# Kernel optimization log

Measured on AMD Instinct MI355X. Metric: run time of the kernel, lower is better.

## Reference

```python
import jax, jax.numpy as jnp
import numpy as np

T, B = 4096, 32
EP_LEN = 256
K = T // EP_LEN          # episodes per trajectory
LM = EP_LEN              # max episode length
S_DIM, C_DIM, M_DIM, L_DIM = 128, 32, 32, 32
E_S, E_C, H, A = 128, 64, 256, 16


def setup_inputs() -> dict:
    key = jax.random.key(0)
    ks = jax.random.split(key, 16)
    f = lambda i, shape: jax.random.normal(ks[i], shape, jnp.float32)
    inp = {
        "state": f(0, (T, B, S_DIM)),
        "latent_mean": f(1, (T, B, L_DIM)) * 0.1,
        "latent_logvar": f(2, (T, B, L_DIM)) * 0.1,
        "latent_mean_t": f(3, (T, B, L_DIM)) * 0.1,
        "latent_logvar_t": f(4, (T, B, L_DIM)) * 0.1,
        "agent_character": f(5, (T, B, C_DIM)),
        "mental_state": f(6, (T, B, M_DIM)),
        "partner_actions": jax.random.randint(ks[7], (LM, B), 0, A, jnp.int32),
    }
    # episode boundaries: done at the last step of each EP_LEN-long episode
    t = jnp.arange(T)
    inp["dones"] = jnp.broadcast_to(((t + 1) % EP_LEN == 0).astype(jnp.float32)[:, None], (T, B))
    sc = lambda fan: 1.0 / np.sqrt(fan)
    inp["W_se"] = f(8, (S_DIM, E_S)) * sc(S_DIM); inp["b_se"] = jnp.zeros((E_S,), jnp.float32)
    inp["W_ce"] = f(9, (C_DIM, E_C)) * sc(C_DIM); inp["b_ce"] = jnp.zeros((E_C,), jnp.float32)
    inp["W_sa"] = f(10, (E_S + E_C, H)) * sc(E_S + E_C); inp["b_sa"] = jnp.zeros((H,), jnp.float32)
    inp["W_h"] = f(11, (E_C + M_DIM, H)) * sc(E_C + M_DIM); inp["b_h"] = jnp.zeros((H,), jnp.float32)
    inp["Wi"] = f(12, (H, 3 * H)) * sc(H); inp["bi"] = jnp.zeros((3 * H,), jnp.float32)
    inp["Wh"] = f(13, (H, 3 * H)) * sc(H); inp["bh"] = jnp.zeros((3 * H,), jnp.float32)
    inp["W_out"] = f(14, (H, A)) * sc(H); inp["b_out"] = jnp.zeros((A,), jnp.float32)
    return inp


def _gru(h, x, Wi, bi, Wh, bh):
    gi = x @ Wi + bi
    gh = h @ Wh + bh
    ir, iz, inn = jnp.split(gi, 3, axis=-1)
    hr, hz, hn = jnp.split(gh, 3, axis=-1)
    r = jax.nn.sigmoid(ir + hr)
    z = jax.nn.sigmoid(iz + hz)
    n = jnp.tanh(inn + r * hn)
    return (1.0 - z) * n + z * h


def _episode_layout(d):  # d: [T] float dones -> (episode_id, pos_in_episode)
    started = jnp.concatenate([jnp.zeros((1,), bool), d[:-1] > 0.5])
    ep = jnp.cumsum(started.astype(jnp.int32))
    t = jnp.arange(d.shape[0])
    start = jax.lax.cummax(jnp.where(started, t, 0))
    return ep, t - start


def _to_episodes(x, ep, pos):  # x: [T, F] -> [K, LM, F]  (transform_timestep_to_batch)
    return jnp.zeros((K, LM) + x.shape[1:], x.dtype).at[ep, pos].set(x, mode="drop")


def _shift_padding_to_front(out, mask):  # out: [K, LM, D], mask: [K, LM]
    cnt = mask.sum(-1).astype(jnp.int32)
    src = jnp.arange(LM)[None, :] - (LM - cnt)[:, None]
    idx = jnp.clip(src, 0, LM - 1)
    ok = (src >= 0).astype(out.dtype)
    shifted = jnp.take_along_axis(out, idx[:, :, None], axis=1) * ok[:, :, None]
    return shifted, jnp.take_along_axis(mask, idx, axis=1) * ok


def _forward(state, latent_mean, latent_logvar, latent_mean_t, latent_logvar_t,
             agent_character, mental_state, partner_actions, dones,
             W_se, b_se, W_ce, b_ce, W_sa, b_sa, W_h, b_h, Wi, bi, Wh, bh, W_out, b_out):
    # ---- KL between consecutive-timestep posteriors ----
    lm = jnp.concatenate((latent_mean, latent_mean_t), axis=-1)
    lv = jnp.concatenate((latent_logvar, latent_logvar_t), axis=-1)
    gauss_dim = lm.shape[-1]
    all_m = jnp.concatenate((jnp.zeros((1,) + lm.shape[1:], lm.dtype), lm), axis=0)
    all_lv = jnp.concatenate((jnp.zeros((1,) + lv.shape[1:], lv.dtype), lv), axis=0)
    mu, m = all_m[1:], all_m[:-1]
    logE, logS = all_lv[1:], all_lv[:-1]
    kl = 0.5 * (jnp.sum(logS, -1) - jnp.sum(logE, -1) - gauss_dim
                + jnp.sum(jnp.exp(logE - logS), -1)
                + jnp.sum((m - mu) * (m - mu) / jnp.exp(logS), -1))  # [T,B]
    kl_loss = kl.sum(0).sum(0).mean()

    # ---- embeddings ----
    se = jax.nn.relu(state @ W_se + b_se)                         # [T,B,E_S]
    ce = jax.nn.relu(agent_character @ W_ce + b_ce)               # [T,B,E_C]
    sa = jnp.concatenate((se, ce), -1) @ W_sa + b_sa              # [T,B,H]
    hid = jnp.concatenate((ce, mental_state), -1) @ W_h + b_h     # [T,B,H]

    # ---- split trajectories into episodes (gather/scatter) ----
    ep, pos = jax.vmap(_episode_layout, in_axes=1, out_axes=0)(dones)  # [B,T] each
    to_ep = jax.vmap(_to_episodes, in_axes=(1, 0, 0), out_axes=0)
    k_sa = to_ep(sa, ep, pos)                                     # [B,K,LM,H]
    k_hid = to_ep(hid, ep, pos)                                   # [B,K,LM,H]
    k_d = to_ep(dones[..., None], ep, pos)[..., 0]                # [B,K,LM]
    mask = jax.vmap(lambda e, p: jnp.zeros((K, LM), jnp.float32).at[e, p].set(1.0, mode="drop"))(ep, pos)

    # ---- sequential RNN scan per episode (vectorized over B*K) ----
    h0 = k_hid[:, :, 0, :]                                        # [B,K,H]
    xs = (jnp.moveaxis(k_sa, 2, 0), jnp.moveaxis(k_hid, 2, 0), jnp.moveaxis(k_d, 2, 0))

    def step(h, xt):
        sa_t, hid_t, d_t = xt
        h = jnp.where(d_t[..., None] > 0.5, hid_t, h)             # reset to per-step init on done
        h = _gru(h, sa_t, Wi, bi, Wh, bh)
        return h, h

    _, ys = jax.lax.scan(step, h0, xs)                            # [LM,B,K,H]
    ys = jnp.moveaxis(ys, 0, 2)                                   # [B,K,LM,H]

    logits = (ys @ W_out + b_out) * mask[..., None]               # [B,K,LM,A]
    shifted, _ = jax.vmap(_shift_padding_to_front)(logits, mask)
    out = jnp.moveaxis(shifted.sum(1), 0, 1)                      # [LM,B,A]

    logp = jnp.take_along_axis(jax.nn.log_softmax(out, -1), partner_actions[..., None], -1)[..., 0]
    return kl_loss, logp.sum(-1)                                  # scalar, [LM]


def reference(state, latent_mean, latent_logvar, latent_mean_t, latent_logvar_t,
              agent_character, mental_state, partner_actions, dones,
              W_se, b_se, W_ce, b_ce, W_sa, b_sa, W_h, b_h, Wi, bi, Wh, bh, W_out, b_out):
    return _forward(state, latent_mean, latent_logvar, latent_mean_t, latent_logvar_t,
                    agent_character, mental_state, partner_actions, dones,
                    W_se, b_se, W_ce, b_ce, W_sa, b_sa, W_h, b_h, Wi, bi, Wh, bh, W_out, b_out)
```

## Files before the change

### kernel.cpp

```cpp
#include <hip/hip_runtime.h>
#include <math.h>

typedef short bf16x8 __attribute__((ext_vector_type(8)));
typedef float f32x4 __attribute__((ext_vector_type(4)));
typedef unsigned short u16;
typedef unsigned int u32;

#define T_DIM 4096
#define B_DIM 32

static constexpr size_t OFF_SE     = 0;
static constexpr size_t OFF_CE     = 33554432;
static constexpr size_t OFF_SA     = 50331648;
static constexpr size_t OFF_HID    = 117440512;
static constexpr size_t OFF_WHT    = 117964800;
static constexpr size_t OFF_WIT    = 118358016;
static constexpr size_t OFF_OUTACC = 118751232;
static constexpr size_t OFF_KLP    = 119799808;

__device__ __forceinline__ u16 f2bf(float x) {
    u32 b = __float_as_uint(x);
    u32 lsb = (b >> 16) & 1u;
    b += 0x7fffu + lsb;
    return (u16)(b >> 16);
}
__device__ __forceinline__ float bf2f(u16 u) {
    return __uint_as_float(((u32)u) << 16);
}
__device__ __forceinline__ float fsig(float x) {
    x = fminf(fmaxf(x, -30.f), 30.f);
    float e = __expf(x);
    return __fdividef(e, e + 1.f);
}
__device__ __forceinline__ float ftanh(float x) {
    x = fminf(fmaxf(x, -15.f), 15.f);
    float e = __expf(2.f * x);
    return __fdividef(e - 1.f, e + 1.f);
}

__global__ __launch_bounds__(256) void prep_kernel(const float* __restrict__ Wh,
                                                   const float* __restrict__ Wi,
                                                   u16* __restrict__ WhT,
                                                   u16* __restrict__ WiT) {
    int idx = blockIdx.x * 256 + threadIdx.x;
    if (idx < 196608) {
        int n = idx >> 8, k = idx & 255;
        WhT[idx] = f2bf(Wh[k * 768 + n]);
    } else {
        int i = idx - 196608;
        int n = i >> 8, k = i & 255;
        WiT[i] = f2bf(Wi[k * 768 + n]);
    }
}

#define KLTERM(MU, LE, M, LS)                   \
    do {                                        \
        float _ls = (LS), _le = (LE);           \
        sS += _ls; sE += _le;                   \
        float _es = expf(-_ls);                 \
        sX += expf(_le) * _es;                  \
        float _dm = (M) - (MU);                 \
        sQ += _dm * _dm * _es;                  \
    } while (0)

__global__ __launch_bounds__(256) void kl_kernel(const float* __restrict__ lm,
                                                 const float* __restrict__ lv,
                                                 const float* __restrict__ lmt,
                                                 const float* __restrict__ lvt,
                                                 float* __restrict__ klp) {
    __shared__ float red[256];
    int tid = threadIdx.x;
    int idx = blockIdx.x * 256 + tid;
    float sS = 0.f, sE = 0.f, sX = 0.f, sQ = 0.f;
    const int cur = idx * 32;
    const int prv = cur - B_DIM * 32;
    const bool hasprev = (idx >= B_DIM);
    for (int half = 0; half < 2; half++) {
        const float* pm = half ? lmt : lm;
        const float* pv = half ? lvt : lv;
        for (int ch = 0; ch < 8; ch++) {
            float4 mu = *(const float4*)&pm[cur + ch * 4];
            float4 le = *(const float4*)&pv[cur + ch * 4];
            float4 m = make_float4(0.f, 0.f, 0.f, 0.f);
            float4 ls = make_float4(0.f, 0.f, 0.f, 0.f);
            if (hasprev) {
                m = *(const float4*)&pm[prv + ch * 4];
                ls = *(const float4*)&pv[prv + ch * 4];
            }
            KLTERM(mu.x, le.x, m.x, ls.x);
            KLTERM(mu.y, le.y, m.y, ls.y);
            KLTERM(mu.z, le.z, m.z, ls.z);
            KLTERM(mu.w, le.w, m.w, ls.w);
        }
    }
    float kl = 0.5f * (sS - sE - 64.0f + sX + sQ);
    red[tid] = kl;
    __syncthreads();
    for (int s = 128; s > 0; s >>= 1) {
        if (tid < s) red[tid] += red[tid + s];
        __syncthreads();
    }
    if (tid == 0) klp[blockIdx.x] = red[0];
}

__global__ __launch_bounds__(256) void gemm_k(const float* __restrict__ A32a,
                                              const u16* __restrict__ A16a,
                                              const u16* __restrict__ A16b,
                                              const float* __restrict__ W,
                                              const float* __restrict__ bias,
                                              u16* __restrict__ out,
                                              int mode, int K, int N, int do_relu) {
    __shared__ __align__(16) u16 As[64 * 40];
    __shared__ __align__(16) u16 Bs[64 * 40];
    const int tid = threadIdx.x;
    const int rows0 = blockIdx.x * 64;
    const int cols0 = blockIdx.y * 64;
    const int w16 = tid >> 6;
    const int lane = tid & 63;
    const int quad = lane >> 4;
    const int l15 = lane & 15;
    f32x4 acc[4];
    for (int i = 0; i < 4; i++) acc[i] = (f32x4){0.f, 0.f, 0.f, 0.f};
    const int nsteps = K >> 5;
    const int arow = tid >> 2, aseg = (tid & 3) << 3;
    const int bk = tid >> 3, bseg = (tid & 7) << 3;
    for (int ks = 0; ks < nsteps; ks++) {
        const int grow = rows0 + arow;
        for (int j = 0; j < 8; j++) {
            const int k = ks * 32 + aseg + j;
            float v;
            if (mode == 0)      v = A32a[grow * 128 + k];
            else if (mode == 1) v = A32a[grow * 32 + k];
            else if (mode == 2) v = (k < 128) ? bf2f(A16a[grow * 128 + k])
                                              : bf2f(A16b[grow * 64 + (k - 128)]);
            else {
                const int k6 = grow >> 6, w = (grow >> 5) & 1, bb = grow & 31;
                const int trow = (k6 * 256 + w * 255) * B_DIM + bb;
                v = (k < 64) ? bf2f(A16a[trow * 64 + k]) : A32a[trow * 32 + (k - 64)];
            }
            As[arow * 40 + aseg + j] = f2bf(v);
        }
        const int gk = ks * 32 + bk;
        for (int j = 0; j < 8; j++) {
            const int c = cols0 + bseg + j;
            Bs[(bseg + j) * 40 + bk] = f2bf(W[gk * N + c]);
        }
        __syncthreads();
        bf16x8 af = *(const bf16x8*)&As[(w16 * 16 + l15) * 40 + quad * 8];
        for (int nt = 0; nt < 4; nt++) {
            bf16x8 bfr = *(const bf16x8*)&Bs[(nt * 16 + l15) * 40 + quad * 8];
            acc[nt] = __builtin_amdgcn_mfma_f32_16x16x32_bf16(af, bfr, acc[nt], 0, 0, 0);
        }
        __syncthreads();
    }
    for (int nt = 0; nt < 4; nt++) {
        const int c = cols0 + nt * 16 + l15;
        const float bv = bias[c];
        for (int r = 0; r < 4; r++) {
            const int row = rows0 + w16 * 16 + quad * 4 + r;
            float v = acc[nt][r] + bv;
            if (do_relu) v = fmaxf(v, 0.f);
            out[row * N + c] = f2bf(v);
        }
    }
}

__global__ void __launch_bounds__(256)
__attribute__((amdgpu_waves_per_eu(1, 1)))
gru5_kernel(const u16* __restrict__ hid,
            const u16* __restrict__ sa,
            const u16* __restrict__ WhT,
            const u16* __restrict__ WiT,
            const float* __restrict__ Wout,
            const float* __restrict__ bi,
            const float* __restrict__ bh,
            u16* __restrict__ gic_all,
            float* __restrict__ outacc) {
    __shared__ __align__(16) u16 whL[12 * 16 * 264];
    __shared__ __align__(16) u16 stage[64 * 264];
    __shared__ __align__(16) u16 hB[16 * 264];
    __shared__ __align__(16) u16 WoL[16 * 264];
    __shared__ float bfold[768];
    __shared__ float bhnL[256];
    const int blk = blockIdx.x;
    const int b = blk >> 1, half = blk & 1;
    const int tid = threadIdx.x;
    const int lane = tid & 63, wv = tid >> 6;
    const int quad = lane >> 4, l15 = lane & 15;
    const int sq = tid >> 5, c0 = (tid & 31) * 8;
    u16* gic = gic_all + (size_t)blk * (256 * 768);

    for (int i = tid; i < 6144; i += 256) {
        const int s = i >> 9, rr = (i >> 5) & 15, seg = (i & 31) * 8;
        const int g = (s / 3) * 12 + 9 + (s % 3);
        *(bf16x8*)&whL[(s * 16 + rr) * 264 + seg] = *(const bf16x8*)&WhT[(g * 16 + rr) * 256 + seg];
    }
    for (int i = tid; i < 4096; i += 256) {
        const int a = i >> 8, k = i & 255;
        WoL[a * 264 + k] = f2bf(Wout[k * 16 + a]);
    }
    for (int c = tid; c < 768; c += 256) bfold[c] = (c < 512) ? (bi[c] + bh[c]) : bi[c];
    if (tid < 256) bhnL[tid] = bh[512 + tid];
    float hreg[8];
    {
        bf16x8 hv = *(const bf16x8*)&hid[(size_t)((((half << 3) + sq) << 6) + b) * 256 + c0];
#pragma unroll
        for (int j = 0; j < 8; j++) hreg[j] = bf2f((u16)hv[j]);
        *(bf16x8*)&hB[sq * 264 + c0] = hv;
        bf16x8 z = (bf16x8){0, 0, 0, 0, 0, 0, 0, 0};
        *(bf16x8*)&hB[(8 + sq) * 264 + c0] = z;
    }
    __syncthreads();

    bf16x8 wreg[9][8];
    for (int ch = 0; ch < 8; ch++) {
        for (int as = 0; as < 4; as++) {
            __syncthreads();
#pragma unroll
            for (int j = 0; j < 8; j++) {
                const int lin = j * 256 + tid;
                const int row = lin >> 5, seg = (lin & 31) * 8;
                const int pcs = as * 8 + (row >> 3), sql = row & 7;
                const int t = ((half << 3) + sql) * 256 + ch * 32 + pcs;
                *(bf16x8*)&stage[row * 264 + seg] =
                    *(const bf16x8*)&sa[((size_t)(t * 32 + b)) * 256 + seg];
            }
            __syncthreads();
            bf16x8 afr[4][8];
#pragma unroll
            for (int mt = 0; mt < 4; mt++)
#pragma unroll
                for (int ks = 0; ks < 8; ks++)
                    afr[mt][ks] = *(const bf16x8*)&stage[(mt * 16 + l15) * 264 + ks * 32 + quad * 8];
            bf16x8 wc[8], wn[8];
            {
                const u16* p = &WiT[((wv * 12) * 16 + l15) * 256 + quad * 8];
#pragma unroll
                for (int ks = 0; ks < 8; ks++) wc[ks] = *(const bf16x8*)&p[ks * 32];
            }
            for (int j = 0; j < 12; j++) {
                if (j < 11) {
                    const u16* p = &WiT[((wv * 12 + j + 1) * 16 + l15) * 256 + quad * 8];
#pragma unroll
                    for (int ks = 0; ks < 8; ks++) wn[ks] = *(const bf16x8*)&p[ks * 32];
                }
                const float bf = bfold[(wv * 12 + j) * 16 + l15];
#pragma unroll
                for (int mt = 0; mt < 4; mt++) {
                    f32x4 acc = (f32x4){0.f, 0.f, 0.f, 0.f};
#pragma unroll
                    for (int ks = 0; ks < 8; ks++)
                        acc = __builtin_amdgcn_mfma_f32_16x16x32_bf16(afr[mt][ks], wc[ks], acc, 0, 0, 0);
                    const int rbase = as * 64 + mt * 16 + quad * 4;
#pragma unroll
                    for (int r = 0; r < 4; r++)
                        gic[(size_t)(rbase + r) * 768 + (wv * 12 + j) * 16 + l15] = f2bf(acc[r] + bf);
                }
#pragma unroll
                for (int ks = 0; ks < 8; ks++) wc[ks] = wn[ks];
            }
        }
#pragma unroll
        for (int j = 0; j < 9; j++) {
            const u16* p = &WhT[((wv * 12 + j) * 16 + l15) * 256 + quad * 8];
#pragma unroll
            for (int ks = 0; ks < 8; ks++) wreg[j][ks] = *(const bf16x8*)&p[ks * 32];
        }
        for (int pc = 0; pc < 32; pc++) {
            const int POS = ch * 32 + pc;
            __syncthreads();
            const u16* gp = &gic[(size_t)(pc * 8 + sq) * 768];
            bf16x8 g_r = *(const bf16x8*)&gp[c0];
            bf16x8 g_z = *(const bf16x8*)&gp[256 + c0];
            bf16x8 g_n = *(const bf16x8*)&gp[512 + c0];
            bf16x8 af[8];
            if (POS == 255) {
                const u16* hp = &hid[(size_t)((((half << 3) + (l15 & 7)) << 6) + 32 + b) * 256 + quad * 8];
#pragma unroll
                for (int ks = 0; ks < 8; ks++) af[ks] = *(const bf16x8*)&hp[ks * 32];
            } else {
#pragma unroll
                for (int ks = 0; ks < 8; ks++)
                    af[ks] = *(const bf16x8*)&hB[l15 * 264 + ks * 32 + quad * 8];
            }
            if (wv == 3 && POS > 0) {
                f32x4 acc = (f32x4){0.f, 0.f, 0.f, 0.f};
#pragma unroll
                for (int ks = 0; ks < 8; ks++) {
                    bf16x8 al = *(const bf16x8*)&hB[l15 * 264 + ks * 32 + quad * 8];
                    bf16x8 wo = *(const bf16x8*)&WoL[l15 * 264 + ks * 32 + quad * 8];
                    acc = __builtin_amdgcn_mfma_f32_16x16x32_bf16(al, wo, acc, 0, 0, 0);
                }
                float s = acc[0] + acc[1] + acc[2] + acc[3];
                s += __shfl_down(s, 32);
                s += __shfl_down(s, 16);
                if (lane < 16)
                    outacc[(size_t)half * 131072 + ((size_t)(POS - 1) * B_DIM + b) * 16 + lane] = s;
            }
#pragma unroll
            for (int j = 0; j < 9; j++) {
                f32x4 acc = (f32x4){0.f, 0.f, 0.f, 0.f};
#pragma unroll
                for (int ks = 0; ks < 8; ks++)
                    acc = __builtin_amdgcn_mfma_f32_16x16x32_bf16(af[ks], wreg[j][ks], acc, 0, 0, 0);
                const int t = wv * 12 + j;
#pragma unroll
                for (int r = 0; r < 4; r++)
                    stage[(quad * 4 + r) * 776 + t * 16 + l15] = f2bf(acc[r]);
            }
#pragma unroll
            for (int j = 9; j < 12; j++) {
                const u16* p = &whL[((wv * 3 + (j - 9)) * 16 + l15) * 264 + quad * 8];
                f32x4 acc = (f32x4){0.f, 0.f, 0.f, 0.f};
#pragma unroll
                for (int ks = 0; ks < 8; ks++)
                    acc = __builtin_amdgcn_mfma_f32_16x16x32_bf16(af[ks], *(const bf16x8*)&p[ks * 32], acc, 0, 0, 0);
                const int t = wv * 12 + j;
#pragma unroll
                for (int r = 0; r < 4; r++)
                    stage[(quad * 4 + r) * 776 + t * 16 + l15] = f2bf(acc[r]);
            }
            __syncthreads();
            if (POS == 255) {
                bf16x8 hv = *(const bf16x8*)&hid[(size_t)((((half << 3) + sq) << 6) + 32 + b) * 256 + c0];
#pragma unroll
                for (int j = 0; j < 8; j++) hreg[j] = bf2f((u16)hv[j]);
            }
            bf16x8 h_r = *(const bf16x8*)&stage[sq * 776 + c0];
            bf16x8 h_z = *(const bf16x8*)&stage[sq * 776 + 256 + c0];
            bf16x8 h_n = *(const bf16x8*)&stage[sq * 776 + 512 + c0];
            bf16x8 hp8;
#pragma unroll
            for (int j = 0; j < 8; j++) {
                const float rv = fsig(bf2f((u16)g_r[j]) + bf2f((u16)h_r[j]));
                const float zv = fsig(bf2f((u16)g_z[j]) + bf2f((u16)h_z[j]));
                const float nv = ftanh(bf2f((u16)g_n[j]) + rv * (bf2f((u16)h_n[j]) + bhnL[c0 + j]));
                hreg[j] = (1.f - zv) * nv + zv * hreg[j];
                hp8[j] = (short)f2bf(hreg[j]);
            }
            *(bf16x8*)&hB[sq * 264 + c0] = hp8;
        }
    }
    __syncthreads();
    if (wv == 3) {
        f32x4 acc = (f32x4){0.f, 0.f, 0.f, 0.f};
#pragma unroll
        for (int ks = 0; ks < 8; ks++) {
            bf16x8 al = *(const bf16x8*)&hB[l15 * 264 + ks * 32 + quad * 8];
            bf16x8 wo = *(const bf16x8*)&WoL[l15 * 264 + ks * 32 + quad * 8];
            acc = __builtin_amdgcn_mfma_f32_16x16x32_bf16(al, wo, acc, 0, 0, 0);
        }
        float s = acc[0] + acc[1] + acc[2] + acc[3];
        s += __shfl_down(s, 32);
        s += __shfl_down(s, 16);
        if (lane < 16)
            outacc[(size_t)half * 131072 + ((size_t)255 * B_DIM + b) * 16 + lane] = s;
    }
}

__global__ __launch_bounds__(64) void final_kernel(const float* __restrict__ outacc,
                                                   const int* __restrict__ pa,
                                                   const float* __restrict__ klp,
                                                   const float* __restrict__ bout,
                                                   float* __restrict__ dout) {
    const int lane = threadIdx.x;
    if (blockIdx.x == 256) {
        float s = 0.f;
        for (int j = 0; j < 8; j++) s += klp[lane + 64 * j];
        for (int off = 32; off > 0; off >>= 1) s += __shfl_down(s, off);
        if (lane == 0) dout[0] = s;
        return;
    }
    const int pos = blockIdx.x;
    float lp = 0.f;
    if (lane < 32) {
        const float* r0 = outacc + ((size_t)pos * B_DIM + lane) * 16;
        const float* r1 = r0 + 131072;
        float v[16];
        float mx = -1e30f;
#pragma unroll
        for (int a = 0; a < 16; a++) {
            v[a] = r0[a] + r1[a] + 16.0f * bout[a];
            mx = fmaxf(mx, v[a]);
        }
        float s = 0.f;
#pragma unroll
        for (int a = 0; a < 16; a++) s += expf(v[a] - mx);
        const int ai = pa[pos * B_DIM + lane];
        lp = v[ai] - mx - logf(s);
    }
    for (int off = 16; off > 0; off >>= 1) lp += __shfl_down(lp, off);
    if (lane == 0) dout[1 + pos] = lp;
}

extern "C" void kernel_launch(void* const* d_in, const int* in_sizes, int n_in,
                              void* d_out, int out_size, void* d_ws, size_t ws_size,
                              hipStream_t stream) {
    const float* state = (const float*)d_in[0];
    const float* lm    = (const float*)d_in[1];
    const float* lv    = (const float*)d_in[2];
    const float* lmt   = (const float*)d_in[3];
    const float* lvt   = (const float*)d_in[4];
    const float* ach   = (const float*)d_in[5];
    const float* ms    = (const float*)d_in[6];
    const int*   pa    = (const int*)d_in[7];
    const float* W_se  = (const float*)d_in[9];
    const float* b_se  = (const float*)d_in[10];
    const float* W_ce  = (const float*)d_in[11];
    const float* b_ce  = (const float*)d_in[12];
    const float* W_sa  = (const float*)d_in[13];
    const float* b_sa  = (const float*)d_in[14];
    const float* W_h   = (const float*)d_in[15];
    const float* b_h   = (const float*)d_in[16];
    const float* Wi    = (const float*)d_in[17];
    const float* bi    = (const float*)d_in[18];
    const float* Wh    = (const float*)d_in[19];
    const float* bh    = (const float*)d_in[20];
    const float* Wout  = (const float*)d_in[21];
    const float* bout  = (const float*)d_in[22];

    char* ws = (char*)d_ws;
    u16* se   = (u16*)(ws + OFF_SE);
    u16* ce   = (u16*)(ws + OFF_CE);
    u16* sa   = (u16*)(ws + OFF_SA);
    u16* hid  = (u16*)(ws + OFF_HID);
    u16* WhT  = (u16*)(ws + OFF_WHT);
    u16* WiT  = (u16*)(ws + OFF_WIT);
    float* outacc = (float*)(ws + OFF_OUTACC);
    float* klp    = (float*)(ws + OFF_KLP);
    float* dout   = (float*)d_out;

    prep_kernel<<<1536, 256, 0, stream>>>(Wh, Wi, WhT, WiT);
    kl_kernel<<<512, 256, 0, stream>>>(lm, lv, lmt, lvt, klp);
    gemm_k<<<dim3(2048, 2), 256, 0, stream>>>(state, nullptr, nullptr, W_se, b_se, se, 0, 128, 128, 1);
    gemm_k<<<dim3(2048, 1), 256, 0, stream>>>(ach, nullptr, nullptr, W_ce, b_ce, ce, 1, 32, 64, 1);
    gemm_k<<<dim3(2048, 4), 256, 0, stream>>>(nullptr, se, ce, W_sa, b_sa, sa, 2, 192, 256, 0);
    gemm_k<<<dim3(16, 4), 256, 0, stream>>>(ms, ce, nullptr, W_h, b_h, hid, 5, 96, 256, 0);
    gru5_kernel<<<64, 256, 0, stream>>>(hid, sa, WhT, WiT, Wout, bi, bh, se, outacc);
    final_kernel<<<257, 64, 0, stream>>>(outacc, pa, klp, bout, dout);
}
```

Measured before the change: 1.859 ms.

## Run GRU recurrence with 8 waves per block and vectorize GEMM tile loads

```diff
diff --git a/kernel.cpp b/kernel.cpp
--- a/kernel.cpp
+++ b/kernel.cpp
@@ -126,24 +126,44 @@
     const int bk = tid >> 3, bseg = (tid & 7) << 3;
     for (int ks = 0; ks < nsteps; ks++) {
         const int grow = rows0 + arow;
-        for (int j = 0; j < 8; j++) {
-            const int k = ks * 32 + aseg + j;
-            float v;
-            if (mode == 0)      v = A32a[grow * 128 + k];
-            else if (mode == 1) v = A32a[grow * 32 + k];
-            else if (mode == 2) v = (k < 128) ? bf2f(A16a[grow * 128 + k])
-                                              : bf2f(A16b[grow * 64 + (k - 128)]);
-            else {
-                const int k6 = grow >> 6, w = (grow >> 5) & 1, bb = grow & 31;
-                const int trow = (k6 * 256 + w * 255) * B_DIM + bb;
-                v = (k < 64) ? bf2f(A16a[trow * 64 + k]) : A32a[trow * 32 + (k - 64)];
-            }
-            As[arow * 40 + aseg + j] = f2bf(v);
+        const int k0 = ks * 32 + aseg;
+        if (mode == 0) {
+            float4 v0 = *(const float4*)&A32a[grow * 128 + k0];
+            float4 v1 = *(const float4*)&A32a[grow * 128 + k0 + 4];
+            u16* d = &As[arow * 40 + aseg];
+            d[0] = f2bf(v0.x); d[1] = f2bf(v0.y); d[2] = f2bf(v0.z); d[3] = f2bf(v0.w);
+            d[4] = f2bf(v1.x); d[5] = f2bf(v1.y); d[6] = f2bf(v1.z); d[7] = f2bf(v1.w);
+        } else if (mode == 1) {
+            float4 v0 = *(const float4*)&A32a[grow * 32 + k0];
+            float4 v1 = *(const float4*)&A32a[grow * 32 + k0 + 4];
+            u16* d = &As[arow * 40 + aseg];
+            d[0] = f2bf(v0.x); d[1] = f2bf(v0.y); d[2] = f2bf(v0.z); d[3] = f2bf(v0.w);
+            d[4] = f2bf(v1.x); d[5] = f2bf(v1.y); d[6] = f2bf(v1.z); d[7] = f2bf(v1.w);
+        } else if (mode == 2) {
+            bf16x8 v = (k0 < 128) ? *(const bf16x8*)&A16a[grow * 128 + k0]
+                                  : *(const bf16x8*)&A16b[grow * 64 + (k0 - 128)];
+            *(bf16x8*)&As[arow * 40 + aseg] = v;
+        } else {
+            const int k6 = grow >> 6, w = (grow >> 5) & 1, bb = grow & 31;
+            const int trow = (k6 * 256 + w * 255) * B_DIM + bb;
+            for (int j = 0; j < 8; j++) {
+                const int k = k0 + j;
+                float v = (k < 64) ? bf2f(A16a[trow * 64 + k]) : A32a[trow * 32 + (k - 64)];
+                As[arow * 40 + aseg + j] = f2bf(v);
+            }
         }
         const int gk = ks * 32 + bk;
-        for (int j = 0; j < 8; j++) {
-            const int c = cols0 + bseg + j;
-            Bs[(bseg + j) * 40 + bk] = f2bf(W[gk * N + c]);
+        {
+            float4 w0 = *(const float4*)&W[gk * N + cols0 + bseg];
+            float4 w1 = *(const float4*)&W[gk * N + cols0 + bseg + 4];
+            Bs[(bseg + 0) * 40 + bk] = f2bf(w0.x);
+            Bs[(bseg + 1) * 40 + bk] = f2bf(w0.y);
+            Bs[(bseg + 2) * 40 + bk] = f2bf(w0.z);
+            Bs[(bseg + 3) * 40 + bk] = f2bf(w0.w);
+            Bs[(bseg + 4) * 40 + bk] = f2bf(w1.x);
+            Bs[(bseg + 5) * 40 + bk] = f2bf(w1.y);
+            Bs[(bseg + 6) * 40 + bk] = f2bf(w1.z);
+            Bs[(bseg + 7) * 40 + bk] = f2bf(w1.w);
         }
         __syncthreads();
         bf16x8 af = *(const bf16x8*)&As[(w16 * 16 + l15) * 40 + quad * 8];
@@ -165,9 +185,9 @@
     }
 }
 
-__global__ void __launch_bounds__(256)
-__attribute__((amdgpu_waves_per_eu(1, 1)))
-gru5_kernel(const u16* __restrict__ hid,
+__global__ void __launch_bounds__(512)
+__attribute__((amdgpu_waves_per_eu(2, 2)))
+gru6_kernel(const u16* __restrict__ hid,
             const u16* __restrict__ sa,
             const u16* __restrict__ WhT,
             const u16* __restrict__ WiT,
@@ -176,7 +196,7 @@
             const float* __restrict__ bh,
             u16* __restrict__ gic_all,
             float* __restrict__ outacc) {
-    __shared__ __align__(16) u16 whL[12 * 16 * 264];
+    __shared__ __align__(16) u16 whL[8 * 16 * 264];
     __shared__ __align__(16) u16 stage[64 * 264];
     __shared__ __align__(16) u16 hB[16 * 264];
     __shared__ __align__(16) u16 WoL[16 * 264];
@@ -187,38 +207,38 @@
     const int tid = threadIdx.x;
     const int lane = tid & 63, wv = tid >> 6;
     const int quad = lane >> 4, l15 = lane & 15;
-    const int sq = tid >> 5, c0 = (tid & 31) * 8;
+    const int c0 = (tid & 63) * 4;
     u16* gic = gic_all + (size_t)blk * (256 * 768);
 
-    for (int i = tid; i < 6144; i += 256) {
+    for (int i = tid; i < 4096; i += 512) {
         const int s = i >> 9, rr = (i >> 5) & 15, seg = (i & 31) * 8;
-        const int g = (s / 3) * 12 + 9 + (s % 3);
+        const int g = s * 6 + 5;
         *(bf16x8*)&whL[(s * 16 + rr) * 264 + seg] = *(const bf16x8*)&WhT[(g * 16 + rr) * 256 + seg];
     }
-    for (int i = tid; i < 4096; i += 256) {
+    for (int i = tid; i < 4096; i += 512) {
         const int a = i >> 8, k = i & 255;
         WoL[a * 264 + k] = f2bf(Wout[k * 16 + a]);
     }
-    for (int c = tid; c < 768; c += 256) bfold[c] = (c < 512) ? (bi[c] + bh[c]) : bi[c];
+    for (int c = tid; c < 768; c += 512) bfold[c] = (c < 512) ? (bi[c] + bh[c]) : bi[c];
     if (tid < 256) bhnL[tid] = bh[512 + tid];
-    float hreg[8];
+    float hreg[4];
     {
-        bf16x8 hv = *(const bf16x8*)&hid[(size_t)((((half << 3) + sq) << 6) + b) * 256 + c0];
-#pragma unroll
-        for (int j = 0; j < 8; j++) hreg[j] = bf2f((u16)hv[j]);
-        *(bf16x8*)&hB[sq * 264 + c0] = hv;
-        bf16x8 z = (bf16x8){0, 0, 0, 0, 0, 0, 0, 0};
-        *(bf16x8*)&hB[(8 + sq) * 264 + c0] = z;
+        ushort4 hv = *(const ushort4*)&hid[(size_t)((((half << 3) + wv) << 6) + b) * 256 + c0];
+        hreg[0] = bf2f(hv.x); hreg[1] = bf2f(hv.y);
+        hreg[2] = bf2f(hv.z); hreg[3] = bf2f(hv.w);
+        *(ushort4*)&hB[wv * 264 + c0] = hv;
+        ushort4 z = make_ushort4(0, 0, 0, 0);
+        *(ushort4*)&hB[(8 + wv) * 264 + c0] = z;
     }
     __syncthreads();
 
-    bf16x8 wreg[9][8];
+    bf16x8 wreg[5][8];
     for (int ch = 0; ch < 8; ch++) {
         for (int as = 0; as < 4; as++) {
             __syncthreads();
 #pragma unroll
-            for (int j = 0; j < 8; j++) {
-                const int lin = j * 256 + tid;
+            for (int j = 0; j < 4; j++) {
+                const int lin = j * 512 + tid;
                 const int row = lin >> 5, seg = (lin & 31) * 8;
                 const int pcs = as * 8 + (row >> 3), sql = row & 7;
                 const int t = ((half << 3) + sql) * 256 + ch * 32 + pcs;
@@ -234,17 +254,17 @@
                     afr[mt][ks] = *(const bf16x8*)&stage[(mt * 16 + l15) * 264 + ks * 32 + quad * 8];
             bf16x8 wc[8], wn[8];
             {
-                const u16* p = &WiT[((wv * 12) * 16 + l15) * 256 + quad * 8];
+                const u16* p = &WiT[((wv * 6) * 16 + l15) * 256 + quad * 8];
 #pragma unroll
                 for (int ks = 0; ks < 8; ks++) wc[ks] = *(const bf16x8*)&p[ks * 32];
             }
-            for (int j = 0; j < 12; j++) {
-                if (j < 11) {
-                    const u16* p = &WiT[((wv * 12 + j + 1) * 16 + l15) * 256 + quad * 8];
+            for (int j = 0; j < 6; j++) {
+                if (j < 5) {
+                    const u16* p = &WiT[((wv * 6 + j + 1) * 16 + l15) * 256 + quad * 8];
 #pragma unroll
                     for (int ks = 0; ks < 8; ks++) wn[ks] = *(const bf16x8*)&p[ks * 32];
                 }
-                const float bf = bfold[(wv * 12 + j) * 16 + l15];
+                const float bf = bfold[(wv * 6 + j) * 16 + l15];
 #pragma unroll
                 for (int mt = 0; mt < 4; mt++) {
                     f32x4 acc = (f32x4){0.f, 0.f, 0.f, 0.f};
@@ -254,25 +274,25 @@
                     const int rbase = as * 64 + mt * 16 + quad * 4;
 #pragma unroll
                     for (int r = 0; r < 4; r++)
-                        gic[(size_t)(rbase + r) * 768 + (wv * 12 + j) * 16 + l15] = f2bf(acc[r] + bf);
+                        gic[(size_t)(rbase + r) * 768 + (wv * 6 + j) * 16 + l15] = f2bf(acc[r] + bf);
                 }
 #pragma unroll
                 for (int ks = 0; ks < 8; ks++) wc[ks] = wn[ks];
             }
         }
 #pragma unroll
-        for (int j = 0; j < 9; j++) {
-            const u16* p = &WhT[((wv * 12 + j) * 16 + l15) * 256 + quad * 8];
+        for (int j = 0; j < 5; j++) {
+            const u16* p = &WhT[((wv * 6 + j) * 16 + l15) * 256 + quad * 8];
 #pragma unroll
             for (int ks = 0; ks < 8; ks++) wreg[j][ks] = *(const bf16x8*)&p[ks * 32];
         }
         for (int pc = 0; pc < 32; pc++) {
             const int POS = ch * 32 + pc;
             __syncthreads();
-            const u16* gp = &gic[(size_t)(pc * 8 + sq) * 768];
-            bf16x8 g_r = *(const bf16x8*)&gp[c0];
-            bf16x8 g_z = *(const bf16x8*)&gp[256 + c0];
-            bf16x8 g_n = *(const bf16x8*)&gp[512 + c0];
+            const u16* gp = &gic[(size_t)(pc * 8 + wv) * 768];
+            ushort4 g_r = *(const ushort4*)&gp[c0];
+            ushort4 g_z = *(const ushort4*)&gp[256 + c0];
+            ushort4 g_n = *(const ushort4*)&gp[512 + c0];
             bf16x8 af[8];
             if (POS == 255) {
                 const u16* hp = &hid[(size_t)((((half << 3) + (l15 & 7)) << 6) + 32 + b) * 256 + quad * 8];
@@ -283,7 +303,7 @@
                 for (int ks = 0; ks < 8; ks++)
                     af[ks] = *(const bf16x8*)&hB[l15 * 264 + ks * 32 + quad * 8];
             }
-            if (wv == 3 && POS > 0) {
+            if (wv == 7 && POS > 0) {
                 f32x4 acc = (f32x4){0.f, 0.f, 0.f, 0.f};
 #pragma unroll
                 for (int ks = 0; ks < 8; ks++) {
@@ -298,51 +318,55 @@
                     outacc[(size_t)half * 131072 + ((size_t)(POS - 1) * B_DIM + b) * 16 + lane] = s;
             }
 #pragma unroll
-            for (int j = 0; j < 9; j++) {
+            for (int j = 0; j < 5; j++) {
                 f32x4 acc = (f32x4){0.f, 0.f, 0.f, 0.f};
 #pragma unroll
                 for (int ks = 0; ks < 8; ks++)
                     acc = __builtin_amdgcn_mfma_f32_16x16x32_bf16(af[ks], wreg[j][ks], acc, 0, 0, 0);
-                const int t = wv * 12 + j;
+                const int t = wv * 6 + j;
 #pragma unroll
                 for (int r = 0; r < 4; r++)
                     stage[(quad * 4 + r) * 776 + t * 16 + l15] = f2bf(acc[r]);
             }
-#pragma unroll
-            for (int j = 9; j < 12; j++) {
-                const u16* p = &whL[((wv * 3 + (j - 9)) * 16 + l15) * 264 + quad * 8];
+            {
+                const u16* p = &whL[(wv * 16 + l15) * 264 + quad * 8];
                 f32x4 acc = (f32x4){0.f, 0.f, 0.f, 0.f};
 #pragma unroll
                 for (int ks = 0; ks < 8; ks++)
                     acc = __builtin_amdgcn_mfma_f32_16x16x32_bf16(af[ks], *(const bf16x8*)&p[ks * 32], acc, 0, 0, 0);
-                const int t = wv * 12 + j;
+                const int t = wv * 6 + 5;
 #pragma unroll
                 for (int r = 0; r < 4; r++)
                     stage[(quad * 4 + r) * 776 + t * 16 + l15] = f2bf(acc[r]);
             }
             __syncthreads();
             if (POS == 255) {
-                bf16x8 hv = *(const bf16x8*)&hid[(size_t)((((half << 3) + sq) << 6) + 32 + b) * 256 + c0];
-#pragma unroll
-                for (int j = 0; j < 8; j++) hreg[j] = bf2f((u16)hv[j]);
-            }
-            bf16x8 h_r = *(const bf16x8*)&stage[sq * 776 + c0];
-            bf16x8 h_z = *(const bf16x8*)&stage[sq * 776 + 256 + c0];
-            bf16x8 h_n = *(const bf16x8*)&stage[sq * 776 + 512 + c0];
-            bf16x8 hp8;
-#pragma unroll
-            for (int j = 0; j < 8; j++) {
-                const float rv = fsig(bf2f((u16)g_r[j]) + bf2f((u16)h_r[j]));
-                const float zv = fsig(bf2f((u16)g_z[j]) + bf2f((u16)h_z[j]));
-                const float nv = ftanh(bf2f((u16)g_n[j]) + rv * (bf2f((u16)h_n[j]) + bhnL[c0 + j]));
+                ushort4 hv = *(const ushort4*)&hid[(size_t)((((half << 3) + wv) << 6) + 32 + b) * 256 + c0];
+                hreg[0] = bf2f(hv.x); hreg[1] = bf2f(hv.y);
+                hreg[2] = bf2f(hv.z); hreg[3] = bf2f(hv.w);
+            }
+            ushort4 h_r = *(const ushort4*)&stage[wv * 776 + c0];
+            ushort4 h_z = *(const ushort4*)&stage[wv * 776 + 256 + c0];
+            ushort4 h_n = *(const ushort4*)&stage[wv * 776 + 512 + c0];
+            const u16* grp = (const u16*)&g_r; const u16* gzp = (const u16*)&g_z;
+            const u16* gnp = (const u16*)&g_n;
+            const u16* hrp = (const u16*)&h_r; const u16* hzp = (const u16*)&h_z;
+            const u16* hnp = (const u16*)&h_n;
+            ushort4 hp4;
+            u16* ho = (u16*)&hp4;
+#pragma unroll
+            for (int j = 0; j < 4; j++) {
+                const float rv = fsig(bf2f(grp[j]) + bf2f(hrp[j]));
+                const float zv = fsig(bf2f(gzp[j]) + bf2f(hzp[j]));
+                const float nv = ftanh(bf2f(gnp[j]) + rv * (bf2f(hnp[j]) + bhnL[c0 + j]));
                 hreg[j] = (1.f - zv) * nv + zv * hreg[j];
-                hp8[j] = (short)f2bf(hreg[j]);
-            }
-            *(bf16x8*)&hB[sq * 264 + c0] = hp8;
+                ho[j] = f2bf(hreg[j]);
+            }
+            *(ushort4*)&hB[wv * 264 + c0] = hp4;
         }
     }
     __syncthreads();
-    if (wv == 3) {
+    if (wv == 7) {
         f32x4 acc = (f32x4){0.f, 0.f, 0.f, 0.f};
 #pragma unroll
         for (int ks = 0; ks < 8; ks++) {
@@ -436,6 +460,6 @@
     gemm_k<<<dim3(2048, 1), 256, 0, stream>>>(ach, nullptr, nullptr, W_ce, b_ce, ce, 1, 32, 64, 1);
     gemm_k<<<dim3(2048, 4), 256, 0, stream>>>(nullptr, se, ce, W_sa, b_sa, sa, 2, 192, 256, 0);
     gemm_k<<<dim3(16, 4), 256, 0, stream>>>(ms, ce, nullptr, W_h, b_h, hid, 5, 96, 256, 0);
-    gru5_kernel<<<64, 256, 0, stream>>>(hid, sa, WhT, WiT, Wout, bi, bh, se, outacc);
+    gru6_kernel<<<64, 512, 0, stream>>>(hid, sa, WhT, WiT, Wout, bi, bh, se, outacc);
     final_kernel<<<257, 64, 0, stream>>>(outacc, pa, klp, bout, dout);
 }
```

New measurement: 1.672 ms. 10.0% less time.
